# Optimization experiments

Measured on AMD Instinct MI355X. Metric: run time of the kernel, lower is better.

## Reference

```python
import jax, jax.numpy as jnp
import numpy as np

EMB = 1024
HEADS = 16
DH = EMB // HEADS


def setup_inputs() -> dict:
    key = jax.random.key(0)
    ks = jax.random.split(key, 9)
    B, S = 4, 2048
    scale = 1.0 / np.sqrt(EMB)
    x = jax.random.normal(ks[0], (B, S, EMB), dtype=jnp.float32)
    Wq = jax.random.normal(ks[1], (EMB, EMB), dtype=jnp.float32) * scale
    Wk = jax.random.normal(ks[2], (EMB, EMB), dtype=jnp.float32) * scale
    Wv = jax.random.normal(ks[3], (EMB, EMB), dtype=jnp.float32) * scale
    Wo = jax.random.normal(ks[4], (EMB, EMB), dtype=jnp.float32) * scale
    bq = jnp.zeros((EMB,), jnp.float32)
    bk = jnp.zeros((EMB,), jnp.float32)
    bv = jnp.zeros((EMB,), jnp.float32)
    bo = jnp.zeros((EMB,), jnp.float32)
    return {"x": x, "Wq": Wq, "bq": bq, "Wk": Wk, "bk": bk,
            "Wv": Wv, "bv": bv, "Wo": Wo, "bo": bo}


def _split_heads(t):
    B, S, _ = t.shape
    return t.reshape(B, S, HEADS, DH).transpose(0, 2, 1, 3)  # [B,H,S,Dh]


def reference(x, Wq, bq, Wk, bk, Wv, bv, Wo, bo):
    q = _split_heads(x @ Wq + bq)
    k = _split_heads(x @ Wk + bk)
    v = _split_heads(x @ Wv + bv)
    # scaled dot-product attention, full [B,H,S,S] score matrix as in source
    logits = jnp.einsum("bhqd,bhkd->bhqk", q, k) / jnp.sqrt(jnp.float32(DH))
    attn = jax.nn.softmax(logits, axis=-1)
    ctx = jnp.einsum("bhqk,bhkd->bhqd", attn, v)
    B, _, S, _ = ctx.shape
    concat = ctx.transpose(0, 2, 1, 3).reshape(B, S, EMB)
    return concat @ Wo + bo
```

## Files before the change

kernel.cpp:

```cpp
#include <hip/hip_runtime.h>
#include <hip/hip_bf16.h>
#include <stdint.h>

typedef __bf16 bf16;
typedef __bf16 bf16x4 __attribute__((ext_vector_type(4)));
typedef __bf16 bf16x8 __attribute__((ext_vector_type(8)));
typedef float f32x4 __attribute__((ext_vector_type(4)));

__device__ __forceinline__ void async_ld16(const void* g, void* l) {
  __builtin_amdgcn_global_load_lds(
      (__attribute__((address_space(1))) void*)(void*)(g),
      (__attribute__((address_space(3))) void*)(l), 16, 0, 0);
}

__global__ __launch_bounds__(256) void cast_f32_bf16(const float* __restrict__ in,
                                                     bf16* __restrict__ out, int n) {
  int i = (blockIdx.x * 256 + threadIdx.x) * 4;
  if (i < n) {
    float4 f = *(const float4*)(in + i);
    bf16x4 v = {(bf16)f.x, (bf16)f.y, (bf16)f.z, (bf16)f.w};
    *(bf16x4*)(out + i) = v;
  }
}

__global__ __launch_bounds__(256) void transpose_cast_f32(const float* __restrict__ src,
                                                          bf16* __restrict__ dst,
                                                          int R, int C) {
  __shared__ bf16 tile[64][66];
  int r0 = blockIdx.x * 64, c0 = blockIdx.y * 64;
  size_t zoff = (size_t)blockIdx.z * R * C;
  int t = threadIdx.x;
#pragma unroll
  for (int i = 0; i < 16; ++i) {
    int idx = t + i * 256;
    int r = idx >> 6, c = idx & 63;
    tile[r][c] = (bf16)src[zoff + (size_t)(r0 + r) * C + (c0 + c)];
  }
  __syncthreads();
#pragma unroll
  for (int i = 0; i < 16; ++i) {
    int idx = t + i * 256;
    int c = idx >> 6, r = idx & 63;
    dst[zoff + (size_t)(c0 + c) * R + (r0 + r)] = tile[r][c];
  }
}

__global__ __launch_bounds__(256) void transpose_cast_bf16(const bf16* __restrict__ src,
                                                           bf16* __restrict__ dst,
                                                           int R, int C) {
  __shared__ bf16 tile[64][66];
  int r0 = blockIdx.x * 64, c0 = blockIdx.y * 64;
  size_t zoff = (size_t)blockIdx.z * R * C;
  int t = threadIdx.x;
#pragma unroll
  for (int i = 0; i < 16; ++i) {
    int idx = t + i * 256;
    int r = idx >> 6, c = idx & 63;
    tile[r][c] = src[zoff + (size_t)(r0 + r) * C + (c0 + c)];
  }
  __syncthreads();
#pragma unroll
  for (int i = 0; i < 16; ++i) {
    int idx = t + i * 256;
    int c = idx >> 6, r = idx & 63;
    dst[zoff + (size_t)(c0 + c) * R + (r0 + r)] = tile[r][c];
  }
}

__device__ __forceinline__ void gemm128_mainloop(const bf16* __restrict__ A,
                                                 const bf16* __restrict__ Bt, int K,
                                                 int rowBase, int colBase,
                                                 bf16* As, bf16* Bs,
                                                 f32x4 (&acc)[4][4]) {
  int t = threadIdx.x, lane = t & 63, w = t >> 6;
  int wM = w >> 1, wN = w & 1, quad = lane >> 4, l15 = lane & 15;
  int r_off = lane >> 3;
  int c_sw = (((lane & 7) ^ r_off) << 3);
  int sw = l15 & 7;
  for (int k0 = 0; k0 < K; k0 += 64) {
    __syncthreads();
#pragma unroll
    for (int i = 0; i < 4; ++i) {
      int e = i * 2048 + w * 512;
      int row = (e >> 6) + r_off;
      async_ld16(A + (size_t)(rowBase + row) * K + (k0 + c_sw), As + e);
      async_ld16(Bt + (size_t)(colBase + row) * K + (k0 + c_sw), Bs + e);
    }
    __syncthreads();
#pragma unroll
    for (int ks = 0; ks < 2; ++ks) {
      int co = (((ks * 4 + quad) ^ sw) << 3);
      bf16x8 af[4], bfr[4];
#pragma unroll
      for (int mi = 0; mi < 4; ++mi)
        af[mi] = *(const bf16x8*)(As + (wM * 64 + mi * 16 + l15) * 64 + co);
#pragma unroll
      for (int ni = 0; ni < 4; ++ni)
        bfr[ni] = *(const bf16x8*)(Bs + (wN * 64 + ni * 16 + l15) * 64 + co);
#pragma unroll
      for (int mi = 0; mi < 4; ++mi)
#pragma unroll
        for (int ni = 0; ni < 4; ++ni)
          acc[mi][ni] = __builtin_amdgcn_mfma_f32_16x16x32_bf16(af[mi], bfr[ni], acc[mi][ni], 0, 0, 0);
    }
  }
}

__global__ __launch_bounds__(256) void gemm_qkv(const bf16* __restrict__ X,
                                                const bf16* __restrict__ Wt,
                                                const float* __restrict__ bq,
                                                const float* __restrict__ bk,
                                                const float* __restrict__ bv,
                                                bf16* __restrict__ Qo,
                                                bf16* __restrict__ Ko,
                                                bf16* __restrict__ Vo) {
  __shared__ alignas(16) bf16 As[128 * 64];
  __shared__ alignas(16) bf16 Bs[128 * 64];
  f32x4 acc[4][4];
  f32x4 z = {0.f, 0.f, 0.f, 0.f};
#pragma unroll
  for (int mi = 0; mi < 4; ++mi)
#pragma unroll
    for (int ni = 0; ni < 4; ++ni) acc[mi][ni] = z;
  int rowBase = blockIdx.x * 128, colBase = blockIdx.y * 128;
  gemm128_mainloop(X, Wt, 1024, rowBase, colBase, As, Bs, acc);

  int t = threadIdx.x, lane = t & 63, w = t >> 6;
  int wM = w >> 1, wN = w & 1, quad = lane >> 4, l15 = lane & 15;
  int which = colBase >> 10;
  const float* bias = which == 0 ? bq : (which == 1 ? bk : bv);
  bf16* dst = which == 0 ? Qo : (which == 1 ? Ko : Vo);
  float scale = which == 0 ? 0.125f * 1.44269504f : 1.0f;
#pragma unroll
  for (int mi = 0; mi < 4; ++mi)
#pragma unroll
    for (int ni = 0; ni < 4; ++ni) {
      int n = colBase + wN * 64 + ni * 16 + l15;
      int e = n & 1023;
      int h = e >> 6, d = e & 63;
      float bb = bias[e];
#pragma unroll
      for (int r = 0; r < 4; ++r) {
        int m = rowBase + wM * 64 + mi * 16 + quad * 4 + r;
        int b = m >> 11, s = m & 2047;
        float val = (acc[mi][ni][r] + bb) * scale;
        dst[(((size_t)((b << 4) + h) * 2048 + s) << 6) + d] = (bf16)val;
      }
    }
}

__global__ __launch_bounds__(256) void gemm_out(const bf16* __restrict__ Cb,
                                                const bf16* __restrict__ Wot,
                                                const float* __restrict__ bo,
                                                float* __restrict__ out) {
  __shared__ alignas(16) bf16 As[128 * 64];
  __shared__ alignas(16) bf16 Bs[128 * 64];
  f32x4 acc[4][4];
  f32x4 z = {0.f, 0.f, 0.f, 0.f};
#pragma unroll
  for (int mi = 0; mi < 4; ++mi)
#pragma unroll
    for (int ni = 0; ni < 4; ++ni) acc[mi][ni] = z;
  int rowBase = blockIdx.x * 128, colBase = blockIdx.y * 128;
  gemm128_mainloop(Cb, Wot, 1024, rowBase, colBase, As, Bs, acc);

  int t = threadIdx.x, lane = t & 63, w = t >> 6;
  int wM = w >> 1, wN = w & 1, quad = lane >> 4, l15 = lane & 15;
#pragma unroll
  for (int mi = 0; mi < 4; ++mi)
#pragma unroll
    for (int ni = 0; ni < 4; ++ni) {
      int n = colBase + wN * 64 + ni * 16 + l15;
      float bb = bo[n];
#pragma unroll
      for (int r = 0; r < 4; ++r) {
        int m = rowBase + wM * 64 + mi * 16 + quad * 4 + r;
        out[(size_t)m * 1024 + n] = acc[mi][ni][r] + bb;
      }
    }
}

__global__ __launch_bounds__(256) void attn(const bf16* __restrict__ Q,
                                            const bf16* __restrict__ Kg,
                                            const bf16* __restrict__ Vt,
                                            bf16* __restrict__ ctx) {
  __shared__ alignas(16) bf16 QPs[128 * 64];
  __shared__ alignas(16) bf16 Ks[64 * 64];
  __shared__ alignas(16) bf16 Vs[64 * 64];

  int t = threadIdx.x, lane = t & 63, w = t >> 6;
  int quad = lane >> 4, l15 = lane & 15;
  int r_off = lane >> 3;
  int c_sw = (((lane & 7) ^ r_off) << 3);
  int sw = l15 & 7;
  int bh = blockIdx.y;
  int q0 = blockIdx.x * 128;
  const bf16* Qp = Q + ((size_t)bh * 2048 + q0) * 64;
  const bf16* Kp = Kg + (size_t)bh * 2048 * 64;
  const bf16* Vp = Vt + (size_t)bh * 64 * 2048;

#pragma unroll
  for (int i = 0; i < 4; ++i) {
    int e = i * 2048 + w * 512;
    int row = (e >> 6) + r_off;
    async_ld16(Qp + row * 64 + c_sw, QPs + e);
  }
  __syncthreads();

  bf16x8 qf[2][2];
#pragma unroll
  for (int ks = 0; ks < 2; ++ks)
#pragma unroll
    for (int qi = 0; qi < 2; ++qi)
      qf[ks][qi] = *(const bf16x8*)(QPs + (w * 32 + qi * 16 + l15) * 64 + (((ks * 4 + quad) ^ sw) << 3));

  bf16* Ps = QPs + w * 2048;

  f32x4 o[2][4];
  f32x4 z = {0.f, 0.f, 0.f, 0.f};
  float lpart[2] = {0.f, 0.f};
#pragma unroll
  for (int mi = 0; mi < 2; ++mi)
#pragma unroll
    for (int ni = 0; ni < 4; ++ni) o[mi][ni] = z;

  for (int kt = 0; kt < 2048; kt += 64) {
    __syncthreads();
#pragma unroll
    for (int i = 0; i < 2; ++i) {
      int e = w * 1024 + i * 512;
      int row = (e >> 6) + r_off;
      async_ld16(Kp + (size_t)(kt + row) * 64 + c_sw, Ks + e);
      async_ld16(Vp + (size_t)row * 2048 + kt + c_sw, Vs + e);
    }
    __syncthreads();

    f32x4 sc[4][2];
#pragma unroll
    for (int ki = 0; ki < 4; ++ki)
#pragma unroll
      for (int qi = 0; qi < 2; ++qi) sc[ki][qi] = z;
#pragma unroll
    for (int ks = 0; ks < 2; ++ks) {
      int co = (((ks * 4 + quad) ^ sw) << 3);
      bf16x8 kf[4];
#pragma unroll
      for (int ki = 0; ki < 4; ++ki)
        kf[ki] = *(const bf16x8*)(Ks + (ki * 16 + l15) * 64 + co);
#pragma unroll
      for (int ki = 0; ki < 4; ++ki)
#pragma unroll
        for (int qi = 0; qi < 2; ++qi)
          sc[ki][qi] = __builtin_amdgcn_mfma_f32_16x16x32_bf16(kf[ki], qf[ks][qi], sc[ki][qi], 0, 0, 0);
    }

#pragma unroll
    for (int qi = 0; qi < 2; ++qi)
#pragma unroll
      for (int ki = 0; ki < 4; ++ki) {
        float p0 = __builtin_amdgcn_exp2f(sc[ki][qi][0]);
        float p1 = __builtin_amdgcn_exp2f(sc[ki][qi][1]);
        float p2 = __builtin_amdgcn_exp2f(sc[ki][qi][2]);
        float p3 = __builtin_amdgcn_exp2f(sc[ki][qi][3]);
        lpart[qi] += (p0 + p1) + (p2 + p3);
        bf16x4 pb = {(bf16)p0, (bf16)p1, (bf16)p2, (bf16)p3};
        int cs = (ki * 2 + (quad >> 1)) ^ sw;
        *(bf16x4*)(Ps + (qi * 16 + l15) * 64 + cs * 8 + (quad & 1) * 4) = pb;
      }

    asm volatile("s_waitcnt lgkmcnt(0)" ::: "memory");

#pragma unroll
    for (int ks = 0; ks < 2; ++ks) {
      int co = (((ks * 4 + quad) ^ sw) << 3);
      bf16x8 pf[2], vf[4];
#pragma unroll
      for (int mi = 0; mi < 2; ++mi)
        pf[mi] = *(const bf16x8*)(Ps + (mi * 16 + l15) * 64 + co);
#pragma unroll
      for (int ni = 0; ni < 4; ++ni)
        vf[ni] = *(const bf16x8*)(Vs + (ni * 16 + l15) * 64 + co);
#pragma unroll
      for (int mi = 0; mi < 2; ++mi)
#pragma unroll
        for (int ni = 0; ni < 4; ++ni)
          o[mi][ni] = __builtin_amdgcn_mfma_f32_16x16x32_bf16(pf[mi], vf[ni], o[mi][ni], 0, 0, 0);
    }
  }

  int b = bh >> 4, h = bh & 15;
#pragma unroll
  for (int mi = 0; mi < 2; ++mi) {
    float l = lpart[mi];
    l += __shfl_xor(l, 16, 64);
    l += __shfl_xor(l, 32, 64);
    float rl[4];
#pragma unroll
    for (int r = 0; r < 4; ++r) rl[r] = 1.0f / __shfl(l, quad * 4 + r, 64);
#pragma unroll
    for (int ni = 0; ni < 4; ++ni) {
      int col = h * 64 + ni * 16 + l15;
#pragma unroll
      for (int r = 0; r < 4; ++r) {
        int q = q0 + w * 32 + mi * 16 + quad * 4 + r;
        ctx[(size_t)(b * 2048 + q) * 1024 + col] = (bf16)(o[mi][ni][r] * rl[r]);
      }
    }
  }
}

extern "C" void kernel_launch(void* const* d_in, const int* in_sizes, int n_in,
                              void* d_out, int out_size, void* d_ws, size_t ws_size,
                              hipStream_t stream) {
  const float* x  = (const float*)d_in[0];
  const float* Wq = (const float*)d_in[1];
  const float* bq = (const float*)d_in[2];
  const float* Wk = (const float*)d_in[3];
  const float* bk = (const float*)d_in[4];
  const float* Wv = (const float*)d_in[5];
  const float* bv = (const float*)d_in[6];
  const float* Wo = (const float*)d_in[7];
  const float* bo = (const float*)d_in[8];
  float* out = (float*)d_out;

  char* ws = (char*)d_ws;
  const size_t MB = 1048576;
  bf16* xb  = (bf16*)(ws);
  bf16* Wt  = (bf16*)(ws + 16 * MB);
  bf16* Wot = (bf16*)(ws + 22 * MB);
  bf16* Qb  = (bf16*)(ws + 24 * MB);
  bf16* Kb  = (bf16*)(ws + 40 * MB);
  bf16* Vb  = (bf16*)(ws + 56 * MB);
  bf16* Vtb = (bf16*)(ws + 72 * MB);
  bf16* Cx  = (bf16*)(ws + 88 * MB);

  cast_f32_bf16<<<8192, 256, 0, stream>>>(x, xb, 8388608);
  transpose_cast_f32<<<dim3(16, 16, 1), 256, 0, stream>>>(Wq, Wt, 1024, 1024);
  transpose_cast_f32<<<dim3(16, 16, 1), 256, 0, stream>>>(Wk, Wt + 1024 * 1024, 1024, 1024);
  transpose_cast_f32<<<dim3(16, 16, 1), 256, 0, stream>>>(Wv, Wt + 2 * 1024 * 1024, 1024, 1024);
  transpose_cast_f32<<<dim3(16, 16, 1), 256, 0, stream>>>(Wo, Wot, 1024, 1024);
  gemm_qkv<<<dim3(64, 24, 1), 256, 0, stream>>>(xb, Wt, bq, bk, bv, Qb, Kb, Vb);
  transpose_cast_bf16<<<dim3(32, 1, 64), 256, 0, stream>>>(Vb, Vtb, 2048, 64);
  attn<<<dim3(16, 64, 1), 256, 0, stream>>>(Qb, Kb, Vtb, Cx);
  gemm_out<<<dim3(64, 8, 1), 256, 0, stream>>>(Cx, Wot, bo, out);
}
```

Measured before the change: 305.3 us.

## Fuse V transpose into QKV GEMM epilogue, merge weight transposes, use fast bf16 packing

The QKV GEMM epilogue now writes V directly in transposed [B,H,D,S] layout with packed 8-byte stores, removing the separate V transpose kernel and its round trip through global memory. The four weight transpose launches are merged into one grid using blockIdx.z. Float-to-bf16 conversions use a round-half-up bit trick with v_perm packing instead of the compiler's round-to-nearest-even conversion. This changes rounding slightly and drops NaN handling in exchange for fewer instructions.

```diff
diff --git a/kernel.cpp b/kernel.cpp
--- a/kernel.cpp
+++ b/kernel.cpp
@@ -11,6 +11,18 @@
   __builtin_amdgcn_global_load_lds(
       (__attribute__((address_space(1))) void*)(void*)(g),
       (__attribute__((address_space(3))) void*)(l), 16, 0, 0);
+}
+
+__device__ __forceinline__ bf16 fast_bf16(float f) {
+  uint32_t u = (__float_as_uint(f) + 0x8000u) >> 16;
+  union { uint16_t s; bf16 b; } cv;
+  cv.s = (uint16_t)u;
+  return cv.b;
+}
+
+__device__ __forceinline__ uint32_t pack_bf16(float lo, float hi) {
+  return __builtin_amdgcn_perm(__float_as_uint(hi) + 0x8000u,
+                               __float_as_uint(lo) + 0x8000u, 0x07060302u);
 }
 
 __global__ __launch_bounds__(256) void cast_f32_bf16(const float* __restrict__ in,
@@ -18,52 +30,37 @@
   int i = (blockIdx.x * 256 + threadIdx.x) * 4;
   if (i < n) {
     float4 f = *(const float4*)(in + i);
-    bf16x4 v = {(bf16)f.x, (bf16)f.y, (bf16)f.z, (bf16)f.w};
-    *(bf16x4*)(out + i) = v;
-  }
-}
-
-__global__ __launch_bounds__(256) void transpose_cast_f32(const float* __restrict__ src,
-                                                          bf16* __restrict__ dst,
-                                                          int R, int C) {
+    uint2 o;
+    o.x = pack_bf16(f.x, f.y);
+    o.y = pack_bf16(f.z, f.w);
+    *(uint2*)(out + i) = o;
+  }
+}
+
+__global__ __launch_bounds__(256) void transpose_weights(const float* __restrict__ Wq,
+                                                         const float* __restrict__ Wk,
+                                                         const float* __restrict__ Wv,
+                                                         const float* __restrict__ Wo,
+                                                         bf16* __restrict__ Wt,
+                                                         bf16* __restrict__ Wot) {
   __shared__ bf16 tile[64][66];
+  int z = blockIdx.z;
+  const float* src = z == 0 ? Wq : (z == 1 ? Wk : (z == 2 ? Wv : Wo));
+  bf16* dst = z == 0 ? Wt : (z == 1 ? Wt + 1048576 : (z == 2 ? Wt + 2097152 : Wot));
   int r0 = blockIdx.x * 64, c0 = blockIdx.y * 64;
-  size_t zoff = (size_t)blockIdx.z * R * C;
   int t = threadIdx.x;
 #pragma unroll
   for (int i = 0; i < 16; ++i) {
     int idx = t + i * 256;
     int r = idx >> 6, c = idx & 63;
-    tile[r][c] = (bf16)src[zoff + (size_t)(r0 + r) * C + (c0 + c)];
+    tile[r][c] = fast_bf16(src[(size_t)(r0 + r) * 1024 + (c0 + c)]);
   }
   __syncthreads();
 #pragma unroll
   for (int i = 0; i < 16; ++i) {
     int idx = t + i * 256;
     int c = idx >> 6, r = idx & 63;
-    dst[zoff + (size_t)(c0 + c) * R + (r0 + r)] = tile[r][c];
-  }
-}
-
-__global__ __launch_bounds__(256) void transpose_cast_bf16(const bf16* __restrict__ src,
-                                                           bf16* __restrict__ dst,
-                                                           int R, int C) {
-  __shared__ bf16 tile[64][66];
-  int r0 = blockIdx.x * 64, c0 = blockIdx.y * 64;
-  size_t zoff = (size_t)blockIdx.z * R * C;
-  int t = threadIdx.x;
-#pragma unroll
-  for (int i = 0; i < 16; ++i) {
-    int idx = t + i * 256;
-    int r = idx >> 6, c = idx & 63;
-    tile[r][c] = src[zoff + (size_t)(r0 + r) * C + (c0 + c)];
-  }
-  __syncthreads();
-#pragma unroll
-  for (int i = 0; i < 16; ++i) {
-    int idx = t + i * 256;
-    int c = idx >> 6, r = idx & 63;
-    dst[zoff + (size_t)(c0 + c) * R + (r0 + r)] = tile[r][c];
+    dst[(size_t)(c0 + c) * 1024 + (r0 + r)] = tile[r][c];
   }
 }
 
@@ -113,7 +110,7 @@
                                                 const float* __restrict__ bv,
                                                 bf16* __restrict__ Qo,
                                                 bf16* __restrict__ Ko,
-                                                bf16* __restrict__ Vo) {
+                                                bf16* __restrict__ Vto) {
   __shared__ alignas(16) bf16 As[128 * 64];
   __shared__ alignas(16) bf16 Bs[128 * 64];
   f32x4 acc[4][4];
@@ -128,25 +125,44 @@
   int t = threadIdx.x, lane = t & 63, w = t >> 6;
   int wM = w >> 1, wN = w & 1, quad = lane >> 4, l15 = lane & 15;
   int which = colBase >> 10;
-  const float* bias = which == 0 ? bq : (which == 1 ? bk : bv);
-  bf16* dst = which == 0 ? Qo : (which == 1 ? Ko : Vo);
-  float scale = which == 0 ? 0.125f * 1.44269504f : 1.0f;
-#pragma unroll
-  for (int mi = 0; mi < 4; ++mi)
-#pragma unroll
-    for (int ni = 0; ni < 4; ++ni) {
-      int n = colBase + wN * 64 + ni * 16 + l15;
-      int e = n & 1023;
-      int h = e >> 6, d = e & 63;
-      float bb = bias[e];
-#pragma unroll
-      for (int r = 0; r < 4; ++r) {
-        int m = rowBase + wM * 64 + mi * 16 + quad * 4 + r;
-        int b = m >> 11, s = m & 2047;
-        float val = (acc[mi][ni][r] + bb) * scale;
-        dst[(((size_t)((b << 4) + h) * 2048 + s) << 6) + d] = (bf16)val;
-      }
-    }
+
+  if (which == 2) {
+#pragma unroll
+    for (int mi = 0; mi < 4; ++mi)
+#pragma unroll
+      for (int ni = 0; ni < 4; ++ni) {
+        int n = colBase + wN * 64 + ni * 16 + l15;
+        int e = n & 1023;
+        int h = e >> 6, d = e & 63;
+        float bb = bv[e];
+        int m0 = rowBase + wM * 64 + mi * 16 + quad * 4;
+        int b = m0 >> 11, s = m0 & 2047;
+        uint2 pv;
+        pv.x = pack_bf16(acc[mi][ni][0] + bb, acc[mi][ni][1] + bb);
+        pv.y = pack_bf16(acc[mi][ni][2] + bb, acc[mi][ni][3] + bb);
+        *(uint2*)(Vto + (((size_t)((b << 4) + h) * 64 + d) << 11) + s) = pv;
+      }
+  } else {
+    const float* bias = which == 0 ? bq : bk;
+    bf16* dst = which == 0 ? Qo : Ko;
+    float scale = which == 0 ? 0.125f * 1.44269504f : 1.0f;
+#pragma unroll
+    for (int mi = 0; mi < 4; ++mi)
+#pragma unroll
+      for (int ni = 0; ni < 4; ++ni) {
+        int n = colBase + wN * 64 + ni * 16 + l15;
+        int e = n & 1023;
+        int h = e >> 6, d = e & 63;
+        float bb = bias[e];
+#pragma unroll
+        for (int r = 0; r < 4; ++r) {
+          int m = rowBase + wM * 64 + mi * 16 + quad * 4 + r;
+          int b = m >> 11, s = m & 2047;
+          dst[(((size_t)((b << 4) + h) * 2048 + s) << 6) + d] =
+              fast_bf16((acc[mi][ni][r] + bb) * scale);
+        }
+      }
+  }
 }
 
 __global__ __launch_bounds__(256) void gemm_out(const bf16* __restrict__ Cb,
@@ -263,9 +279,11 @@
         float p2 = __builtin_amdgcn_exp2f(sc[ki][qi][2]);
         float p3 = __builtin_amdgcn_exp2f(sc[ki][qi][3]);
         lpart[qi] += (p0 + p1) + (p2 + p3);
-        bf16x4 pb = {(bf16)p0, (bf16)p1, (bf16)p2, (bf16)p3};
+        uint2 pb;
+        pb.x = pack_bf16(p0, p1);
+        pb.y = pack_bf16(p2, p3);
         int cs = (ki * 2 + (quad >> 1)) ^ sw;
-        *(bf16x4*)(Ps + (qi * 16 + l15) * 64 + cs * 8 + (quad & 1) * 4) = pb;
+        *(uint2*)(Ps + (qi * 16 + l15) * 64 + cs * 8 + (quad & 1) * 4) = pb;
       }
 
     asm volatile("s_waitcnt lgkmcnt(0)" ::: "memory");
@@ -303,7 +321,7 @@
 #pragma unroll
       for (int r = 0; r < 4; ++r) {
         int q = q0 + w * 32 + mi * 16 + quad * 4 + r;
-        ctx[(size_t)(b * 2048 + q) * 1024 + col] = (bf16)(o[mi][ni][r] * rl[r]);
+        ctx[(size_t)(b * 2048 + q) * 1024 + col] = fast_bf16(o[mi][ni][r] * rl[r]);
       }
     }
   }
@@ -330,17 +348,12 @@
   bf16* Wot = (bf16*)(ws + 22 * MB);
   bf16* Qb  = (bf16*)(ws + 24 * MB);
   bf16* Kb  = (bf16*)(ws + 40 * MB);
-  bf16* Vb  = (bf16*)(ws + 56 * MB);
-  bf16* Vtb = (bf16*)(ws + 72 * MB);
-  bf16* Cx  = (bf16*)(ws + 88 * MB);
+  bf16* Vtb = (bf16*)(ws + 56 * MB);
+  bf16* Cx  = (bf16*)(ws + 72 * MB);
 
   cast_f32_bf16<<<8192, 256, 0, stream>>>(x, xb, 8388608);
-  transpose_cast_f32<<<dim3(16, 16, 1), 256, 0, stream>>>(Wq, Wt, 1024, 1024);
-  transpose_cast_f32<<<dim3(16, 16, 1), 256, 0, stream>>>(Wk, Wt + 1024 * 1024, 1024, 1024);
-  transpose_cast_f32<<<dim3(16, 16, 1), 256, 0, stream>>>(Wv, Wt + 2 * 1024 * 1024, 1024, 1024);
-  transpose_cast_f32<<<dim3(16, 16, 1), 256, 0, stream>>>(Wo, Wot, 1024, 1024);
-  gemm_qkv<<<dim3(64, 24, 1), 256, 0, stream>>>(xb, Wt, bq, bk, bv, Qb, Kb, Vb);
-  transpose_cast_bf16<<<dim3(32, 1, 64), 256, 0, stream>>>(Vb, Vtb, 2048, 64);
+  transpose_weights<<<dim3(16, 16, 4), 256, 0, stream>>>(Wq, Wk, Wv, Wo, Wt, Wot);
+  gemm_qkv<<<dim3(64, 24, 1), 256, 0, stream>>>(xb, Wt, bq, bk, bv, Qb, Kb, Vtb);
   attn<<<dim3(16, 64, 1), 256, 0, stream>>>(Qb, Kb, Vtb, Cx);
   gemm_out<<<dim3(64, 8, 1), 256, 0, stream>>>(Cx, Wot, bo, out);
 }
```

Result: faster. 298.8 us (-2.1%).
